# Performance work log

Measured on AMD Instinct MI355X. Metric: run time of the kernel, lower is better.

The kernel has to match this reference:

```python
import jax, jax.numpy as jnp
import numpy as np

NUM_EMBEDDINGS = 1024
EMBEDDING_DIM = 128
COMMITMENT_COST = 0.25


def setup_inputs() -> dict:
    key = jax.random.key(0)
    k1, k2 = jax.random.split(key)
    z = jax.random.normal(k1, (16, EMBEDDING_DIM, 64, 64), dtype=jnp.float32)
    # torch init: uniform(-1/num_embeddings, 1/num_embeddings)
    lim = 1.0 / NUM_EMBEDDINGS
    embedding = jax.random.uniform(
        k2, (NUM_EMBEDDINGS, EMBEDDING_DIM), dtype=jnp.float32,
        minval=-lim, maxval=lim)
    return {"z": z, "embedding": embedding}


def reference(z, embedding):
    b, c, h, w = z.shape  # c == EMBEDDING_DIM
    # (b, h, w, c) -> (b*h*w, c)
    z_flat = jnp.transpose(z, (0, 2, 3, 1)).reshape(-1, c)
    # squared euclidean distances: ||z||^2 + ||e||^2 - 2 z e^T  -> (N, K)
    distances = (jnp.sum(z_flat ** 2, axis=-1, keepdims=True)
                 + jnp.sum(embedding ** 2, axis=-1)[None, :]
                 - 2.0 * jnp.matmul(z_flat, embedding.T))
    encoding_indices = jnp.argmin(distances, axis=-1)  # (N,) int
    z_q = embedding[encoding_indices].reshape(b, h, w, c)
    z_q = jnp.transpose(z_q, (0, 3, 1, 2))  # (b, c, h, w)
    commitment_loss = COMMITMENT_COST * jnp.sum(
        (jax.lax.stop_gradient(z_q) - z) ** 2)
    codebook_loss = jnp.sum((z_q - jax.lax.stop_gradient(z)) ** 2)
    loss = codebook_loss + commitment_loss
    # straight-through estimator
    z_q_st = z + jax.lax.stop_gradient(z_q - z)
    return (z_q_st, loss, encoding_indices, commitment_loss, codebook_loss)
```

## Files before the change

kernel.cpp:

```cpp
#include <hip/hip_runtime.h>
#include <hip/hip_bf16.h>

#define C 128
#define HW 4096
#define NPOS 65536
#define K 1024
#define MB 256
#define NBLK (NPOS/MB)
#define RS 136
#define RSB 272
#define CHK 64
#define NCH (K/CHK)
#define CHB (CHK*RSB)

#define ZQ_OFF 0
#define LOSS_OFF 8388608
#define IDX_OFF 8388609
#define COMMIT_OFF 8454145
#define CODE_OFF 8454146

#define WS_IMG_OFF 8192

typedef __bf16 bf16x8 __attribute__((ext_vector_type(8)));
typedef float f32x4 __attribute__((ext_vector_type(4)));
typedef unsigned short u16x8 __attribute__((ext_vector_type(8)));

__global__ void vq_prep(const float* __restrict__ emb, unsigned char* __restrict__ img,
                        float* __restrict__ S) {
    int k = blockIdx.x;
    int l = threadIdx.x;
    if (k == 0 && l == 0) S[0] = 0.0f;
    float v0 = emb[k * C + l];
    float v1 = emb[k * C + 64 + l];
    __hip_bfloat16 h0 = __float2bfloat16(v0);
    __hip_bfloat16 h1 = __float2bfloat16(v1);
    unsigned short* row = (unsigned short*)(img + (size_t)k * RSB);
    row[l] = *(unsigned short*)&h0;
    row[64 + l] = *(unsigned short*)&h1;
    float s = v0 * v0 + v1 * v1;
    #pragma unroll
    for (int off = 32; off; off >>= 1) s += __shfl_down(s, off);
    if (l == 0) *(float*)(img + (size_t)k * RSB + 256) = s + 1.0f;
}

__global__ __launch_bounds__(512)
void vq_main(const float* __restrict__ z, const float* __restrict__ emb,
             const unsigned char* __restrict__ img,
             float* __restrict__ out, float* __restrict__ S) {
    __shared__ __align__(16) unsigned short zt[MB * RS];
    __shared__ __align__(16) unsigned short bbuf[2][CHK * RS];
    __shared__ unsigned int wbest[2][MB];
    __shared__ unsigned short idxs[MB];
    __shared__ float lred[8];

    const int t = threadIdx.x;
    const int w = t >> 6;
    const int lane = t & 63;
    const int nn = lane & 15;
    const int q = lane >> 4;
    const int wm = w >> 1;
    const int wn = w & 1;

    const int blk = blockIdx.x;
    const int n0g = blk * MB;
    const int b = n0g >> 12;
    const int hw0 = n0g & (HW - 1);
    const float* zg = z + (size_t)b * C * HW + hw0;
    unsigned char* ztb = (unsigned char*)zt;

    for (int j = w; j < 17; j += 8) {
        __builtin_amdgcn_global_load_lds(
            (const __attribute__((address_space(1))) unsigned int*)(img + j * 1024 + lane * 16),
            (__attribute__((address_space(3))) unsigned int*)((unsigned char*)bbuf[0] + j * 1024),
            16, 0, 0);
    }

    {
        const int pos4 = (t & 63) * 4;
        const int c0 = (t >> 6) * 16;
        float4 fv[16];
        #pragma unroll
        for (int i = 0; i < 16; ++i)
            fv[i] = *(const float4*)&zg[(size_t)(c0 + i) * HW + pos4];
        #pragma unroll
        for (int j = 0; j < 4; ++j) {
            u16x8 p0, p1;
            #pragma unroll
            for (int i = 0; i < 8; ++i) {
                float f0 = (j == 0) ? fv[i].x : (j == 1) ? fv[i].y
                         : (j == 2) ? fv[i].z : fv[i].w;
                float f1 = (j == 0) ? fv[8 + i].x : (j == 1) ? fv[8 + i].y
                         : (j == 2) ? fv[8 + i].z : fv[8 + i].w;
                __hip_bfloat16 h0 = __float2bfloat16(f0);
                __hip_bfloat16 h1 = __float2bfloat16(f1);
                p0[i] = *(unsigned short*)&h0;
                p1[i] = *(unsigned short*)&h1;
            }
            const unsigned int row = pos4 + j;
            const unsigned int sw = ((row >> 2) & 7u) << 4;
            const unsigned int base = row * RSB + c0 * 2;
            *(u16x8*)(ztb + (base ^ sw)) = p0;
            *(u16x8*)(ztb + ((base + 16) ^ sw)) = p1;
        }
    }
    __syncthreads();

    bf16x8 a[4][4];
    #pragma unroll
    for (int mt = 0; mt < 4; ++mt)
        #pragma unroll
        for (int ks = 0; ks < 4; ++ks) {
            const unsigned int row = wm * 64 + mt * 16 + nn;
            const unsigned int sw = ((row >> 2) & 7u) << 4;
            a[mt][ks] = *(bf16x8*)(ztb + ((row * RSB + ks * 64 + q * 16) ^ sw));
            asm volatile("" : "+v"(*(f32x4*)&a[mt][ks]));
        }

    unsigned int best[4][4];
    #pragma unroll
    for (int mt = 0; mt < 4; ++mt)
        #pragma unroll
        for (int r = 0; r < 4; ++r) best[mt][r] = 0xFFFFFFFFu;

    for (int ch = 0; ch < NCH; ++ch) {
        const int p = ch & 1;
        if (ch + 1 < NCH) {
            const unsigned char* src = img + (size_t)(ch + 1) * CHB;
            for (int j = w; j < 17; j += 8) {
                __builtin_amdgcn_global_load_lds(
                    (const __attribute__((address_space(1))) unsigned int*)(src + j * 1024 + lane * 16),
                    (__attribute__((address_space(3))) unsigned int*)((unsigned char*)bbuf[p ^ 1] + j * 1024),
                    16, 0, 0);
            }
        }
        const unsigned short* bb = bbuf[p];

        const int row0 = wn * 32 + nn;
        const int row1 = row0 + 16;
        bf16x8 bf0[4], bf1[4];
        #pragma unroll
        for (int ks = 0; ks < 4; ++ks) {
            bf0[ks] = *(const bf16x8*)&bb[row0 * RS + ks * 32 + q * 8];
            bf1[ks] = *(const bf16x8*)&bb[row1 * RS + ks * 32 + q * 8];
        }
        const float en0 = *(const float*)&bb[row0 * RS + 128];
        const float en1 = *(const float*)&bb[row1 * RS + 128];
        const unsigned int code0 = (unsigned int)(ch * CHK + wn * 32 + nn);

        f32x4 acc0[4], acc1[4];
        #pragma unroll
        for (int mt = 0; mt < 4; ++mt) {
            acc0[mt] = (f32x4){0.f, 0.f, 0.f, 0.f};
            acc1[mt] = (f32x4){0.f, 0.f, 0.f, 0.f};
        }
        #pragma unroll
        for (int ks = 0; ks < 4; ++ks)
            #pragma unroll
            for (int mt = 0; mt < 4; ++mt) {
                acc0[mt] = __builtin_amdgcn_mfma_f32_16x16x32_bf16(a[mt][ks], bf0[ks], acc0[mt], 0, 0, 0);
                acc1[mt] = __builtin_amdgcn_mfma_f32_16x16x32_bf16(a[mt][ks], bf1[ks], acc1[mt], 0, 0, 0);
            }

        #pragma unroll
        for (int mt = 0; mt < 4; ++mt)
            #pragma unroll
            for (int r = 0; r < 4; ++r) {
                float s0 = fmaf(acc0[mt][r], -2.0f, en0);
                float s1 = fmaf(acc1[mt][r], -2.0f, en1);
                unsigned int u0 = (__float_as_uint(s0) & ~1023u) | code0;
                unsigned int u1 = (__float_as_uint(s1) & ~1023u) | (code0 + 16u);
                best[mt][r] = min(best[mt][r], min(u0, u1));
            }
        __syncthreads();
    }

    #pragma unroll
    for (int mt = 0; mt < 4; ++mt)
        #pragma unroll
        for (int r = 0; r < 4; ++r) {
            unsigned int v = best[mt][r];
            v = min(v, (unsigned int)__shfl_xor((int)v, 1));
            v = min(v, (unsigned int)__shfl_xor((int)v, 2));
            v = min(v, (unsigned int)__shfl_xor((int)v, 4));
            v = min(v, (unsigned int)__shfl_xor((int)v, 8));
            if (nn == 0) wbest[wn][wm * 64 + mt * 16 + q * 4 + r] = v;
        }
    __syncthreads();

    if (t < MB) {
        unsigned int v = min(wbest[0][t], wbest[1][t]);
        unsigned int code = v & 1023u;
        idxs[t] = (unsigned short)code;
        out[IDX_OFF + n0g + t] = (float)code;
    }
    __syncthreads();

    {
        const int pos4 = (t & 63) * 4;
        const int c0 = (t >> 6) * 16;
        float* og = out + ZQ_OFF + (size_t)b * C * HW + hw0;
        float ev[4][16];
        float ls = 0.f;
        #pragma unroll
        for (int j = 0; j < 4; ++j) {
            const int pos = pos4 + j;
            const float* erow = emb + (size_t)idxs[pos] * C;
            #pragma unroll
            for (int g = 0; g < 4; ++g) {
                float4 e = *(const float4*)&erow[c0 + g * 4];
                ev[j][g * 4 + 0] = e.x; ev[j][g * 4 + 1] = e.y;
                ev[j][g * 4 + 2] = e.z; ev[j][g * 4 + 3] = e.w;
            }
            const unsigned int row = (unsigned int)pos;
            const unsigned int sw = ((row >> 2) & 7u) << 4;
            const unsigned int base = row * RSB + c0 * 2;
            u16x8 z0 = *(u16x8*)(ztb + (base ^ sw));
            u16x8 z1 = *(u16x8*)(ztb + ((base + 16) ^ sw));
            #pragma unroll
            for (int i = 0; i < 8; ++i) {
                float zf0 = __uint_as_float((unsigned int)z0[i] << 16);
                float zf1 = __uint_as_float((unsigned int)z1[i] << 16);
                float d0 = zf0 - ev[j][i];
                float d1 = zf1 - ev[j][8 + i];
                ls += d0 * d0 + d1 * d1;
            }
        }
        #pragma unroll
        for (int i = 0; i < 16; ++i) {
            float4 v = { ev[0][i], ev[1][i], ev[2][i], ev[3][i] };
            *(float4*)&og[(size_t)(c0 + i) * HW + pos4] = v;
        }
        #pragma unroll
        for (int off = 32; off; off >>= 1) ls += __shfl_down(ls, off);
        if (lane == 0) lred[w] = ls;
    }
    __syncthreads();
    if (t == 0) {
        float bs = 0.f;
        #pragma unroll
        for (int i = 0; i < 8; ++i) bs += lred[i];
        atomicAdd(S, bs);
    }
}

__global__ void vq_final(const float* __restrict__ S, float* __restrict__ out) {
    float s = *S;
    out[LOSS_OFF] = 1.25f * s;
    out[COMMIT_OFF] = 0.25f * s;
    out[CODE_OFF] = s;
}

extern "C" void kernel_launch(void* const* d_in, const int* in_sizes, int n_in,
                              void* d_out, int out_size, void* d_ws, size_t ws_size,
                              hipStream_t stream) {
    const float* z = (const float*)d_in[0];
    const float* emb = (const float*)d_in[1];
    float* out = (float*)d_out;
    float* S = (float*)d_ws;
    unsigned char* img = (unsigned char*)d_ws + WS_IMG_OFF;

    vq_prep<<<K, 64, 0, stream>>>(emb, img, S);
    vq_main<<<NBLK, 512, 0, stream>>>(z, emb, img, out, S);
    vq_final<<<1, 1, 0, stream>>>(S, out);
}
```

Measured before the change: 118.5 us.

## Double codebook chunk size, drop LDS swizzle, fuse final loss into main kernel

```diff
diff --git a/kernel.cpp b/kernel.cpp
--- a/kernel.cpp
+++ b/kernel.cpp
@@ -9,7 +9,7 @@
 #define NBLK (NPOS/MB)
 #define RS 136
 #define RSB 272
-#define CHK 64
+#define CHK 128
 #define NCH (K/CHK)
 #define CHB (CHK*RSB)
 
@@ -29,7 +29,7 @@
                         float* __restrict__ S) {
     int k = blockIdx.x;
     int l = threadIdx.x;
-    if (k == 0 && l == 0) S[0] = 0.0f;
+    if (k == 0 && l == 0) { S[0] = 0.0f; ((unsigned int*)S)[1] = 0u; }
     float v0 = emb[k * C + l];
     float v1 = emb[k * C + 64 + l];
     __hip_bfloat16 h0 = __float2bfloat16(v0);
@@ -66,9 +66,8 @@
     const int b = n0g >> 12;
     const int hw0 = n0g & (HW - 1);
     const float* zg = z + (size_t)b * C * HW + hw0;
-    unsigned char* ztb = (unsigned char*)zt;
-
-    for (int j = w; j < 17; j += 8) {
+
+    for (int j = w; j < 34; j += 8) {
         __builtin_amdgcn_global_load_lds(
             (const __attribute__((address_space(1))) unsigned int*)(img + j * 1024 + lane * 16),
             (__attribute__((address_space(3))) unsigned int*)((unsigned char*)bbuf[0] + j * 1024),
@@ -96,11 +95,8 @@
                 p0[i] = *(unsigned short*)&h0;
                 p1[i] = *(unsigned short*)&h1;
             }
-            const unsigned int row = pos4 + j;
-            const unsigned int sw = ((row >> 2) & 7u) << 4;
-            const unsigned int base = row * RSB + c0 * 2;
-            *(u16x8*)(ztb + (base ^ sw)) = p0;
-            *(u16x8*)(ztb + ((base + 16) ^ sw)) = p1;
+            *(u16x8*)&zt[(pos4 + j) * RS + c0] = p0;
+            *(u16x8*)&zt[(pos4 + j) * RS + c0 + 8] = p1;
         }
     }
     __syncthreads();
@@ -110,9 +106,7 @@
     for (int mt = 0; mt < 4; ++mt)
         #pragma unroll
         for (int ks = 0; ks < 4; ++ks) {
-            const unsigned int row = wm * 64 + mt * 16 + nn;
-            const unsigned int sw = ((row >> 2) & 7u) << 4;
-            a[mt][ks] = *(bf16x8*)(ztb + ((row * RSB + ks * 64 + q * 16) ^ sw));
+            a[mt][ks] = *(bf16x8*)&zt[(wm * 64 + mt * 16 + nn) * RS + ks * 32 + q * 8];
             asm volatile("" : "+v"(*(f32x4*)&a[mt][ks]));
         }
 
@@ -126,7 +120,7 @@
         const int p = ch & 1;
         if (ch + 1 < NCH) {
             const unsigned char* src = img + (size_t)(ch + 1) * CHB;
-            for (int j = w; j < 17; j += 8) {
+            for (int j = w; j < 34; j += 8) {
                 __builtin_amdgcn_global_load_lds(
                     (const __attribute__((address_space(1))) unsigned int*)(src + j * 1024 + lane * 16),
                     (__attribute__((address_space(3))) unsigned int*)((unsigned char*)bbuf[p ^ 1] + j * 1024),
@@ -135,42 +129,45 @@
         }
         const unsigned short* bb = bbuf[p];
 
-        const int row0 = wn * 32 + nn;
-        const int row1 = row0 + 16;
-        bf16x8 bf0[4], bf1[4];
-        #pragma unroll
-        for (int ks = 0; ks < 4; ++ks) {
-            bf0[ks] = *(const bf16x8*)&bb[row0 * RS + ks * 32 + q * 8];
-            bf1[ks] = *(const bf16x8*)&bb[row1 * RS + ks * 32 + q * 8];
-        }
-        const float en0 = *(const float*)&bb[row0 * RS + 128];
-        const float en1 = *(const float*)&bb[row1 * RS + 128];
-        const unsigned int code0 = (unsigned int)(ch * CHK + wn * 32 + nn);
-
-        f32x4 acc0[4], acc1[4];
-        #pragma unroll
-        for (int mt = 0; mt < 4; ++mt) {
-            acc0[mt] = (f32x4){0.f, 0.f, 0.f, 0.f};
-            acc1[mt] = (f32x4){0.f, 0.f, 0.f, 0.f};
-        }
-        #pragma unroll
-        for (int ks = 0; ks < 4; ++ks)
+        #pragma unroll
+        for (int half = 0; half < 2; ++half) {
+            const int row0 = wn * 64 + half * 32 + nn;
+            const int row1 = row0 + 16;
+            bf16x8 bf0[4], bf1[4];
+            #pragma unroll
+            for (int ks = 0; ks < 4; ++ks) {
+                bf0[ks] = *(const bf16x8*)&bb[row0 * RS + ks * 32 + q * 8];
+                bf1[ks] = *(const bf16x8*)&bb[row1 * RS + ks * 32 + q * 8];
+            }
+            const float en0 = *(const float*)&bb[row0 * RS + 128];
+            const float en1 = *(const float*)&bb[row1 * RS + 128];
+            const unsigned int code0 = (unsigned int)(ch * CHK + wn * 64 + half * 32 + nn);
+
+            f32x4 acc0[4], acc1[4];
             #pragma unroll
             for (int mt = 0; mt < 4; ++mt) {
-                acc0[mt] = __builtin_amdgcn_mfma_f32_16x16x32_bf16(a[mt][ks], bf0[ks], acc0[mt], 0, 0, 0);
-                acc1[mt] = __builtin_amdgcn_mfma_f32_16x16x32_bf16(a[mt][ks], bf1[ks], acc1[mt], 0, 0, 0);
-            }
-
-        #pragma unroll
-        for (int mt = 0; mt < 4; ++mt)
-            #pragma unroll
-            for (int r = 0; r < 4; ++r) {
-                float s0 = fmaf(acc0[mt][r], -2.0f, en0);
-                float s1 = fmaf(acc1[mt][r], -2.0f, en1);
-                unsigned int u0 = (__float_as_uint(s0) & ~1023u) | code0;
-                unsigned int u1 = (__float_as_uint(s1) & ~1023u) | (code0 + 16u);
-                best[mt][r] = min(best[mt][r], min(u0, u1));
-            }
+                acc0[mt] = (f32x4){0.f, 0.f, 0.f, 0.f};
+                acc1[mt] = (f32x4){0.f, 0.f, 0.f, 0.f};
+            }
+            #pragma unroll
+            for (int ks = 0; ks < 4; ++ks)
+                #pragma unroll
+                for (int mt = 0; mt < 4; ++mt) {
+                    acc0[mt] = __builtin_amdgcn_mfma_f32_16x16x32_bf16(a[mt][ks], bf0[ks], acc0[mt], 0, 0, 0);
+                    acc1[mt] = __builtin_amdgcn_mfma_f32_16x16x32_bf16(a[mt][ks], bf1[ks], acc1[mt], 0, 0, 0);
+                }
+
+            #pragma unroll
+            for (int mt = 0; mt < 4; ++mt)
+                #pragma unroll
+                for (int r = 0; r < 4; ++r) {
+                    float s0 = fmaf(acc0[mt][r], -2.0f, en0);
+                    float s1 = fmaf(acc1[mt][r], -2.0f, en1);
+                    unsigned int u0 = (__float_as_uint(s0) & ~1023u) | code0;
+                    unsigned int u1 = (__float_as_uint(s1) & ~1023u) | (code0 + 16u);
+                    best[mt][r] = min(best[mt][r], min(u0, u1));
+                }
+        }
         __syncthreads();
     }
 
@@ -211,11 +208,8 @@
                 ev[j][g * 4 + 0] = e.x; ev[j][g * 4 + 1] = e.y;
                 ev[j][g * 4 + 2] = e.z; ev[j][g * 4 + 3] = e.w;
             }
-            const unsigned int row = (unsigned int)pos;
-            const unsigned int sw = ((row >> 2) & 7u) << 4;
-            const unsigned int base = row * RSB + c0 * 2;
-            u16x8 z0 = *(u16x8*)(ztb + (base ^ sw));
-            u16x8 z1 = *(u16x8*)(ztb + ((base + 16) ^ sw));
+            u16x8 z0 = *(u16x8*)&zt[pos * RS + c0];
+            u16x8 z1 = *(u16x8*)&zt[pos * RS + c0 + 8];
             #pragma unroll
             for (int i = 0; i < 8; ++i) {
                 float zf0 = __uint_as_float((unsigned int)z0[i] << 16);
@@ -235,19 +229,21 @@
         if (lane == 0) lred[w] = ls;
     }
     __syncthreads();
+
     if (t == 0) {
         float bs = 0.f;
         #pragma unroll
         for (int i = 0; i < 8; ++i) bs += lred[i];
-        atomicAdd(S, bs);
-    }
-}
-
-__global__ void vq_final(const float* __restrict__ S, float* __restrict__ out) {
-    float s = *S;
-    out[LOSS_OFF] = 1.25f * s;
-    out[COMMIT_OFF] = 0.25f * s;
-    out[CODE_OFF] = s;
+        float prev = atomicAdd(S, bs);
+        asm volatile("" :: "v"(prev) : "memory");
+        unsigned int old = atomicAdd((unsigned int*)S + 1, 1u);
+        if (old == NBLK - 1) {
+            float s = atomicAdd(S, 0.0f);
+            out[LOSS_OFF] = 1.25f * s;
+            out[COMMIT_OFF] = 0.25f * s;
+            out[CODE_OFF] = s;
+        }
+    }
 }
 
 extern "C" void kernel_launch(void* const* d_in, const int* in_sizes, int n_in,
@@ -261,5 +257,4 @@
 
     vq_prep<<<K, 64, 0, stream>>>(emb, img, S);
     vq_main<<<NBLK, 512, 0, stream>>>(z, emb, img, out, S);
-    vq_final<<<1, 1, 0, stream>>>(S, out);
 }
```

Measured after the change: 117.7 us. About the same (-0.7%).
